# Optimization experiments

Hardware: AMD Instinct MI355X
Metric: run time of the kernel (lower is better)

The kernel has to match this reference:

```python
import jax, jax.numpy as jnp
import numpy as np

BATCH = 65536
FEAT_DIM = 512
NUM_CLASS = 16
LAMDA = 1.0
LAMDA1 = 10.0
SCALE = 1.0
EPS = 1e-9


def setup_inputs() -> dict:
    key = jax.random.key(0)
    k1, k2, k3 = jax.random.split(key, 3)
    output_features = jax.random.normal(k1, (BATCH, FEAT_DIM), dtype=jnp.float32)
    y_truth = jax.random.randint(k2, (BATCH,), 0, NUM_CLASS, dtype=jnp.int64)
    feature_centers = jax.random.normal(k3, (NUM_CLASS, FEAT_DIM), dtype=jnp.float32)
    return {
        "output_features": output_features,
        "y_truth": y_truth,
        "feature_centers": feature_centers,
    }


def reference(output_features, y_truth, feature_centers):
    batch_size = output_features.shape[0]
    factor = SCALE / batch_size

    # Center loss: gather per-sample class center, squared diff, sum.
    centers_batch = feature_centers[y_truth]              # [B, D]
    diff = output_features - centers_batch
    loss_center = 0.5 * jnp.sum(diff * diff) * factor

    # Pairwise cosine similarity over class centers (upper triangle, j<k),
    # replacing the O(C^2) python loop with one matmul + mask + reduce.
    norms = jnp.sqrt(jnp.sum(feature_centers * feature_centers, axis=1))  # [C]
    gram = feature_centers @ feature_centers.T                            # [C, C]
    denom = norms[:, None] * norms[None, :] + EPS
    cos = gram / denom
    c = feature_centers.shape[0]
    upper = jnp.triu(jnp.ones((c, c), dtype=bool), k=1)
    item1_sum = jnp.sum(jnp.where(upper, cos + 1.0, 0.0))

    loss_island = LAMDA * (loss_center + LAMDA1 * item1_sum)
    return loss_island
```

## Files before the change

kernel.cpp:

```cpp
#include <hip/hip_runtime.h>
#include <math.h>

#define BATCH    65536
#define FEAT     512
#define NCLASS   16
#define LAMDA    1.0f
#define LAMDA1   10.0f
#define SCALE    1.0f
#define EPS      1e-9f

constexpr int BLOCK  = 256;
constexpr int GRID   = 4096;
constexpr int NV     = BATCH * (FEAT / 4);
constexpr int STRIDE = GRID * BLOCK;
constexpr int ITERS  = NV / STRIDE;

constexpr int WS_ITEM1 = GRID;

typedef float f4v __attribute__((ext_vector_type(4)));

__global__ __launch_bounds__(BLOCK) void island_main(
    const f4v* __restrict__ x,
    const int* __restrict__ y,
    const f4v* __restrict__ centers4,
    float*     __restrict__ ws)
{
    __shared__ float wsum[4];
    __shared__ float gram[NCLASS][NCLASS];
    __shared__ f4v   xstage[ITERS * BLOCK];

    const int bid  = blockIdx.x;
    const int t    = threadIdx.x;
    const int lane = t & 63;
    const int wid  = t >> 6;

    if (bid < GRID) {
        const int tid = bid * BLOCK + t;

        const int base_b = __builtin_amdgcn_readfirstlane(tid >> 7);
        const int d4     = t & 127;

        int cls[ITERS];
        #pragma unroll
        for (int it = 0; it < ITERS; ++it)
            cls[it] = y[base_b + it * (STRIDE >> 7)];

        #pragma unroll
        for (int it = 0; it < ITERS; ++it) {
            const f4v* g = &x[tid + it * STRIDE];
            f4v*       l = &xstage[it * BLOCK + wid * 64];
            __builtin_amdgcn_global_load_lds(
                (const __attribute__((address_space(1))) void*)g,
                (__attribute__((address_space(3))) void*)l,
                16, 0, 0);
        }
        asm volatile("s_waitcnt vmcnt(0)" ::: "memory");

        float sum = 0.0f;
        #pragma unroll
        for (int it = 0; it < ITERS; ++it) {
            f4v xv = xstage[it * BLOCK + t];
            f4v cv = centers4[cls[it] * (FEAT / 4) + d4];
            f4v e  = xv - cv;
            sum += e.x * e.x + e.y * e.y + e.z * e.z + e.w * e.w;
        }

        #pragma unroll
        for (int off = 32; off > 0; off >>= 1)
            sum += __shfl_down(sum, off, 64);

        if (lane == 0) wsum[wid] = sum;
        __syncthreads();
        if (t == 0)
            ws[bid] = wsum[0] + wsum[1] + wsum[2] + wsum[3];
    } else {
        const int j = t >> 4;
        const int k = t & 15;
        const f4v* cj = centers4 + j * (FEAT / 4);
        const f4v* ck = centers4 + k * (FEAT / 4);
        float dot = 0.0f;
        #pragma unroll 8
        for (int i = 0; i < FEAT / 4; ++i) {
            f4v a = cj[i];
            f4v b = ck[i];
            dot += a.x * b.x + a.y * b.y + a.z * b.z + a.w * b.w;
        }
        gram[j][k] = dot;
        __syncthreads();

        if (t == 0) {
            float item1 = 0.0f;
            for (int jj = 0; jj < NCLASS; ++jj) {
                float nj = sqrtf(gram[jj][jj]);
                for (int kk = jj + 1; kk < NCLASS; ++kk) {
                    float nk = sqrtf(gram[kk][kk]);
                    item1 += gram[jj][kk] / (nj * nk + EPS) + 1.0f;
                }
            }
            ws[WS_ITEM1] = item1;
        }
    }
}

__global__ __launch_bounds__(256) void finalize_kernel(
    const float* __restrict__ ws,
    float*       __restrict__ out)
{
    float psum = 0.0f;
    #pragma unroll
    for (int k = 0; k < GRID / 256; ++k)
        psum += ws[threadIdx.x + k * 256];
    #pragma unroll
    for (int off = 32; off > 0; off >>= 1)
        psum += __shfl_down(psum, off, 64);

    __shared__ float wsum[4];
    const int lane = threadIdx.x & 63;
    const int wid  = threadIdx.x >> 6;
    if (lane == 0) wsum[wid] = psum;
    __syncthreads();

    if (threadIdx.x == 0) {
        float total = wsum[0] + wsum[1] + wsum[2] + wsum[3];
        float loss_center = 0.5f * total * (SCALE / (float)BATCH);
        out[0] = LAMDA * (loss_center + LAMDA1 * ws[WS_ITEM1]);
    }
}

extern "C" void kernel_launch(void* const* d_in, const int* in_sizes, int n_in,
                              void* d_out, int out_size, void* d_ws, size_t ws_size,
                              hipStream_t stream) {
    const float* x       = (const float*)d_in[0];
    const int*   y       = (const int*)d_in[1];
    const float* centers = (const float*)d_in[2];
    float* out = (float*)d_out;
    float* ws  = (float*)d_ws;

    island_main<<<GRID + 1, BLOCK, 0, stream>>>(
        (const f4v*)x, y, (const f4v*)centers, ws);

    finalize_kernel<<<1, 256, 0, stream>>>(ws, out);
}
```

Baseline: 212.7 us.

## Replace LDS-staged loads with nontemporal direct loads and pair logical blocks per workgroup

Removes the global_load_lds staging buffer and reads x directly into registers with nontemporal loads. Each workgroup now handles two logical blocks, halving the launched grid while keeping the same partial-sum layout in the workspace. This drops LDS traffic and the extra waitcnt, and the nontemporal hint is meant to keep streamed data from polluting cache. In exchange it adds register pressure and may reduce memory-level parallelism, since the second pair's loads could be serialized behind the first.

```diff
diff --git a/kernel.cpp b/kernel.cpp
--- a/kernel.cpp
+++ b/kernel.cpp
@@ -10,12 +10,14 @@
 #define EPS      1e-9f
 
 constexpr int BLOCK  = 256;
-constexpr int GRID   = 4096;
+constexpr int OGRID  = 4096;
+constexpr int PAIR   = 2;
+constexpr int GRID2  = OGRID / PAIR;
 constexpr int NV     = BATCH * (FEAT / 4);
-constexpr int STRIDE = GRID * BLOCK;
+constexpr int STRIDE = OGRID * BLOCK;
 constexpr int ITERS  = NV / STRIDE;
 
-constexpr int WS_ITEM1 = GRID;
+constexpr int WS_ITEM1 = OGRID;
 
 typedef float f4v __attribute__((ext_vector_type(4)));
 
@@ -27,52 +29,51 @@
 {
     __shared__ float wsum[4];
     __shared__ float gram[NCLASS][NCLASS];
-    __shared__ f4v   xstage[ITERS * BLOCK];
 
     const int bid  = blockIdx.x;
     const int t    = threadIdx.x;
     const int lane = t & 63;
     const int wid  = t >> 6;
 
-    if (bid < GRID) {
-        const int tid = bid * BLOCK + t;
-
-        const int base_b = __builtin_amdgcn_readfirstlane(tid >> 7);
-        const int d4     = t & 127;
-
-        int cls[ITERS];
-        #pragma unroll
-        for (int it = 0; it < ITERS; ++it)
-            cls[it] = y[base_b + it * (STRIDE >> 7)];
+    if (bid < GRID2) {
+        const int d4 = t & 127;
+        float sums[PAIR];
 
         #pragma unroll
-        for (int it = 0; it < ITERS; ++it) {
-            const f4v* g = &x[tid + it * STRIDE];
-            f4v*       l = &xstage[it * BLOCK + wid * 64];
-            __builtin_amdgcn_global_load_lds(
-                (const __attribute__((address_space(1))) void*)g,
-                (__attribute__((address_space(3))) void*)l,
-                16, 0, 0);
-        }
-        asm volatile("s_waitcnt vmcnt(0)" ::: "memory");
+        for (int p = 0; p < PAIR; ++p) {
+            const int lb  = bid + p * GRID2;
+            const int tid = lb * BLOCK + t;
 
-        float sum = 0.0f;
-        #pragma unroll
-        for (int it = 0; it < ITERS; ++it) {
-            f4v xv = xstage[it * BLOCK + t];
-            f4v cv = centers4[cls[it] * (FEAT / 4) + d4];
-            f4v e  = xv - cv;
-            sum += e.x * e.x + e.y * e.y + e.z * e.z + e.w * e.w;
+            const int base_b = __builtin_amdgcn_readfirstlane(tid >> 7);
+
+            int cls[ITERS];
+            #pragma unroll
+            for (int it = 0; it < ITERS; ++it)
+                cls[it] = y[base_b + it * (STRIDE >> 7)];
+
+            float sum = 0.0f;
+            #pragma unroll
+            for (int it = 0; it < ITERS; ++it) {
+                f4v xv = __builtin_nontemporal_load(&x[tid + it * STRIDE]);
+                f4v cv = centers4[cls[it] * (FEAT / 4) + d4];
+                f4v e  = xv - cv;
+                sum += e.x * e.x + e.y * e.y + e.z * e.z + e.w * e.w;
+            }
+            sums[p] = sum;
         }
 
         #pragma unroll
-        for (int off = 32; off > 0; off >>= 1)
-            sum += __shfl_down(sum, off, 64);
-
-        if (lane == 0) wsum[wid] = sum;
-        __syncthreads();
-        if (t == 0)
-            ws[bid] = wsum[0] + wsum[1] + wsum[2] + wsum[3];
+        for (int p = 0; p < PAIR; ++p) {
+            float sum = sums[p];
+            #pragma unroll
+            for (int off = 32; off > 0; off >>= 1)
+                sum += __shfl_down(sum, off, 64);
+            if (lane == 0) wsum[wid] = sum;
+            __syncthreads();
+            if (t == 0)
+                ws[bid + p * GRID2] = wsum[0] + wsum[1] + wsum[2] + wsum[3];
+            __syncthreads();
+        }
     } else {
         const int j = t >> 4;
         const int k = t & 15;
@@ -108,7 +109,7 @@
 {
     float psum = 0.0f;
     #pragma unroll
-    for (int k = 0; k < GRID / 256; ++k)
+    for (int k = 0; k < OGRID / 256; ++k)
         psum += ws[threadIdx.x + k * 256];
     #pragma unroll
     for (int off = 32; off > 0; off >>= 1)
@@ -136,7 +137,7 @@
     float* out = (float*)d_out;
     float* ws  = (float*)d_ws;
 
-    island_main<<<GRID + 1, BLOCK, 0, stream>>>(
+    island_main<<<GRID2 + 1, BLOCK, 0, stream>>>(
         (const f4v*)x, y, (const f4v*)centers, ws);
 
     finalize_kernel<<<1, 256, 0, stream>>>(ws, out);
```

Measured after the change: 201.0 us, median of 2. 5.5% less time.
